# Kernel optimization log

Hardware: AMD Instinct MI355X
Metric: run time of the kernel (lower is better)

## Reference

```python
import jax, jax.numpy as jnp
import numpy as np

NUM_HEADS = 12
HEAD_DIM = 64
DROPKEY = 0.1
BN_EPS = 1e-5


def setup_inputs() -> dict:
    key = jax.random.key(0)
    ks = jax.random.split(key, 6)
    b, n, d = 4, 1024, 768
    img_c, hw = 256, 32
    x = jax.random.normal(ks[0], (b, n, d), dtype=jnp.float32)
    y = jax.random.normal(ks[1], (b, img_c, hw, hw), dtype=jnp.float32)
    drop_mask = jax.random.uniform(ks[2], (b, NUM_HEADS, n, n), dtype=jnp.float32)
    W_qkv = jax.random.normal(ks[3], (d, 3 * d), dtype=jnp.float32) * (d ** -0.5)
    conv1_w = jax.random.normal(ks[4], (img_c, 1, 3, 3), dtype=jnp.float32) * 0.1
    conv2_w = jax.random.normal(ks[5], (d, img_c, 1, 1), dtype=jnp.float32) * (img_c ** -0.5)
    bn_gamma = jnp.ones((d,), dtype=jnp.float32)
    bn_beta = jnp.zeros((d,), dtype=jnp.float32)
    return {"x": x, "y": y, "drop_mask": drop_mask, "W_qkv": W_qkv,
            "conv1_w": conv1_w, "conv2_w": conv2_w,
            "bn_gamma": bn_gamma, "bn_beta": bn_beta}


def reference(x, y, drop_mask, W_qkv, conv1_w, conv2_w, bn_gamma, bn_beta):
    b, n, d = x.shape
    h, hd = NUM_HEADS, HEAD_DIM
    scale = hd ** -0.5

    # --- attention branch ---
    qkv = x @ W_qkv                                     # [b, n, 3d]
    q, k, v = jnp.split(qkv, 3, axis=-1)
    def to_heads(t):
        return t.reshape(b, n, h, hd).transpose(0, 2, 1, 3)  # [b, h, n, hd]
    q, k, v = to_heads(q), to_heads(k), to_heads(v)
    scores = jnp.einsum('bhid,bhjd->bhij', q, k) * scale
    # dropkey: bernoulli(p) additive -1e12 mask before softmax
    mask = (drop_mask < DROPKEY).astype(scores.dtype)
    scores = scores + mask * jnp.asarray(-1e12, scores.dtype)
    attn = jax.nn.softmax(scores, axis=-1)
    out = jnp.einsum('bhij,bhjd->bhid', attn, v)        # [b, h, n, hd]
    out = out.transpose(0, 2, 1, 3).reshape(b, n, h * hd)

    # --- conv branch: depthwise 3x3 -> 1x1 -> BN(train) -> ReLU ---
    img_c = y.shape[1]
    y1 = jax.lax.conv_general_dilated(
        y, conv1_w, window_strides=(1, 1), padding='SAME',
        dimension_numbers=('NCHW', 'OIHW', 'NCHW'),
        feature_group_count=img_c)                      # [b, img_c, H, W]
    y2 = jax.lax.conv_general_dilated(
        y1, conv2_w, window_strides=(1, 1), padding='SAME',
        dimension_numbers=('NCHW', 'OIHW', 'NCHW'))     # [b, d, H, W]
    mean = jnp.mean(y2, axis=(0, 2, 3), keepdims=True)
    var = jnp.var(y2, axis=(0, 2, 3), keepdims=True)
    y_bn = (y2 - mean) * jax.lax.rsqrt(var + BN_EPS)
    y_bn = y_bn * bn_gamma[None, :, None, None] + bn_beta[None, :, None, None]
    y_out = jax.nn.relu(y_bn)                           # [b, d, H, W]

    # patchify(p1=p2=1) + flatten == 'b c h w -> b (h w) c'
    y_tok = y_out.transpose(0, 2, 3, 1).reshape(b, n, d)
    return (out + y_tok, y_out)


if __name__ == '__main__':
    inp = setup_inputs()
    o, yo = jax.jit(reference)(**inp)
    print(o.shape, yo.shape)
```

## Files before the change

kernel.cpp:

```cpp
#include <hip/hip_runtime.h>
#include <cstddef>

#define B_     4
#define NTOK   1024
#define DMODEL 768
#define NH     12
#define IMGC   256
#define NPIX   1024

typedef __attribute__((ext_vector_type(8))) short bf16x8;
typedef __attribute__((ext_vector_type(4))) float f32x4;
typedef __attribute__((ext_vector_type(8))) unsigned short u16x8;

static __device__ __forceinline__ unsigned short f2bf(float f) {
  unsigned int u = __float_as_uint(f);
  u += 0x7FFFu + ((u >> 16) & 1u);
  return (unsigned short)(u >> 16);
}

#define SWZ(row, b) (((row) << 7) + ((b) ^ (((row) & 7) << 4)))

#define GLOAD16(g, l) __builtin_amdgcn_global_load_lds(                      \
    (const __attribute__((address_space(1))) void*)(g),                      \
    (__attribute__((address_space(3))) void*)(l), 16, 0, 0)

__global__ __launch_bounds__(256) void k_cvt(const float* __restrict__ X,
                                             const float* __restrict__ Wqkv,
                                             const float* __restrict__ W2,
                                             const float* __restrict__ Yimg,
                                             const float* __restrict__ w1,
                                             unsigned short* __restrict__ Xb,
                                             unsigned short* __restrict__ Wtb,
                                             unsigned short* __restrict__ W2b,
                                             float* __restrict__ y1,
                                             float* __restrict__ bnacc) {
  __shared__ unsigned short T[32][33];
  const int bid = blockIdx.x;
  const int t = threadIdx.x;
  if (bid < 1536) {
    const size_t i8 = (size_t)bid * 256 + t;
    const float4 a = *(const float4*)(X + i8 * 8);
    const float4 b = *(const float4*)(X + i8 * 8 + 4);
    u16x8 o;
    o[0] = f2bf(a.x); o[1] = f2bf(a.y); o[2] = f2bf(a.z); o[3] = f2bf(a.w);
    o[4] = f2bf(b.x); o[5] = f2bf(b.y); o[6] = f2bf(b.z); o[7] = f2bf(b.w);
    *(u16x8*)(Xb + i8 * 8) = o;
  } else if (bid < 3264) {
    const int b2 = bid - 1536;
    const int n0 = (b2 % 72) * 32, k0 = (b2 / 72) * 32;
    const int tx = t & 31, ty = t >> 5;
#pragma unroll
    for (int i = 0; i < 4; i++) {
      int kl = ty + i * 8;
      T[tx][kl] = f2bf(Wqkv[(size_t)(k0 + kl) * 2304 + n0 + tx]);
    }
    __syncthreads();
#pragma unroll
    for (int i = 0; i < 4; i++) {
      int nl = ty + i * 8;
      Wtb[(size_t)(n0 + nl) * 768 + k0 + tx] = T[nl][tx];
    }
  } else if (bid < 3360) {
    const size_t i8 = (size_t)(bid - 3264) * 256 + t;
    const float4 a = *(const float4*)(W2 + i8 * 8);
    const float4 b = *(const float4*)(W2 + i8 * 8 + 4);
    u16x8 o;
    o[0] = f2bf(a.x); o[1] = f2bf(a.y); o[2] = f2bf(a.z); o[3] = f2bf(a.w);
    o[4] = f2bf(b.x); o[5] = f2bf(b.y); o[6] = f2bf(b.z); o[7] = f2bf(b.w);
    *(u16x8*)(W2b + i8 * 8) = o;
  } else if (bid == 3360) {
    for (int i = t; i < 1536; i += 256) bnacc[i] = 0.0f;
  } else {
    const int bc = bid - 3361;
    const int c = bc & 255;
    const float* yin = Yimg + (size_t)bc * NPIX;
    float* yout = y1 + (size_t)bc * NPIX;
    float w[9];
#pragma unroll
    for (int i = 0; i < 9; i++) w[i] = w1[c * 9 + i];
#pragma unroll
    for (int rep = 0; rep < 4; rep++) {
      int px = t + rep * 256;
      int yy = px >> 5, xx = px & 31;
      float acc = 0.0f;
#pragma unroll
      for (int dy = -1; dy <= 1; dy++) {
        int sy = yy + dy;
        if (sy < 0 || sy > 31) continue;
#pragma unroll
        for (int dx = -1; dx <= 1; dx++) {
          int sx = xx + dx;
          if (sx < 0 || sx > 31) continue;
          acc = fmaf(yin[(sy << 5) + sx], w[(dy + 1) * 3 + dx + 1], acc);
        }
      }
      yout[px] = acc;
    }
  }
}

__global__ __launch_bounds__(256) void k_qkv_gemm(const unsigned short* __restrict__ Xb,
                                                  const unsigned short* __restrict__ Wt,
                                                  unsigned short* __restrict__ q,
                                                  unsigned short* __restrict__ k,
                                                  unsigned short* __restrict__ v) {
  __shared__ __align__(16) char AsB[16384];
  __shared__ __align__(16) char BsB[16384];
  const int t = threadIdx.x;
  const int w = t >> 6, l = t & 63;
  const int r = l & 15, g = l >> 4;
  const int wr = w >> 1, wc = w & 1;
  const int m0 = blockIdx.y * 128;
  const int n0 = blockIdx.x * 128;
  const int rsel  = l >> 3;
  const int slotp = (l & 7) ^ (rsel & 7);
  f32x4 acc[4][4] = {};

  for (int step = 0; step < 12; ++step) {
    const int k0 = step * 64;
#pragma unroll
    for (int i = 0; i < 4; i++) {
      const int chunk = (i << 2) + w;
      const int row = (chunk << 3) + rsel;
      GLOAD16(Xb + (size_t)(m0 + row) * 768 + k0 + (slotp << 3),
              AsB + (chunk << 10) + (l << 4));
      GLOAD16(Wt + (size_t)(n0 + row) * 768 + k0 + (slotp << 3),
              BsB + (chunk << 10) + (l << 4));
    }
    __syncthreads();
#pragma unroll
    for (int kk = 0; kk < 2; kk++) {
      bf16x8 a[4], b[4];
#pragma unroll
      for (int m = 0; m < 4; m++) {
        const int row = wr * 64 + m * 16 + r;
        a[m] = *(const bf16x8*)(AsB + SWZ(row, kk * 64 + (g << 4)));
      }
#pragma unroll
      for (int n = 0; n < 4; n++) {
        const int row = wc * 64 + n * 16 + r;
        b[n] = *(const bf16x8*)(BsB + SWZ(row, kk * 64 + (g << 4)));
      }
#pragma unroll
      for (int m = 0; m < 4; m++)
#pragma unroll
        for (int n = 0; n < 4; n++)
          acc[m][n] = __builtin_amdgcn_mfma_f32_16x16x32_bf16(a[m], b[n], acc[m][n], 0, 0, 0);
    }
    __syncthreads();
  }

  const int which = blockIdx.x / 6;
  const int cbase = (blockIdx.x - which * 6) * 128 + wc * 64;
  unsigned short* dst = which == 0 ? q : (which == 1 ? k : v);
#pragma unroll
  for (int m = 0; m < 4; m++) {
    const int grow = m0 + wr * 64 + m * 16 + g * 4;
#pragma unroll
    for (int n = 0; n < 4; n++) {
      const int c = cbase + n * 16 + r;
      const int head = c >> 6, dim = c & 63;
#pragma unroll
      for (int reg = 0; reg < 4; reg++) {
        const int row = grow + reg;
        const int bb = row >> 10, tok = row & 1023;
        dst[((size_t)(((bb * NH + head) << 10) + tok) << 6) + dim] = f2bf(acc[m][n][reg]);
      }
    }
  }
}

__global__ __launch_bounds__(256) void k_attn(const unsigned short* __restrict__ qb,
                                              const unsigned short* __restrict__ kb,
                                              const unsigned short* __restrict__ vb,
                                              const float* __restrict__ dm,
                                              const float* __restrict__ y2,
                                              const float* __restrict__ bn_sum,
                                              const float* __restrict__ bn_sumsq,
                                              const float* __restrict__ gamma,
                                              const float* __restrict__ beta,
                                              float* __restrict__ out0) {
  __shared__ __align__(16) unsigned short QsA[4096];
  __shared__ __align__(16) unsigned short KsA[4096];
  __shared__ __align__(16) unsigned short VtA[4096];
  __shared__ __align__(16) unsigned short PsA[4096];
  char* qs = (char*)QsA; char* ks = (char*)KsA;
  char* vt = (char*)VtA; char* ps = (char*)PsA;
  const int bh = blockIdx.x;
  const int qt = blockIdx.y;
  const int t  = threadIdx.x;
  const int w = t >> 6, l = t & 63, r = l & 15, g = l >> 4;
  const size_t hbase = (size_t)bh << 16;
  const char* qg = (const char*)(qb + hbase + ((size_t)qt << 12));
  const char* kg = (const char*)(kb + hbase);
  const char* vg = (const char*)(vb + hbase);
  const float* mp = dm + ((size_t)bh << 20) + ((size_t)(qt * 64) << 10);

#pragma unroll
  for (int i = 0; i < 2; i++) {
    int cid = t + (i << 8);
    int row = cid >> 3, slot = cid & 7;
    uint4 val = *(const uint4*)(qg + row * 128 + slot * 16);
    *(uint4*)(qs + SWZ(row, slot * 16)) = val;
  }

  float m_run[4] = {-INFINITY, -INFINITY, -INFINITY, -INFINITY};
  float l_run[4] = {0.0f, 0.0f, 0.0f, 0.0f};
  f32x4 O[4] = {};

  for (int kt = 0; kt < 16; kt++) {
    __syncthreads();
#pragma unroll
    for (int i = 0; i < 2; i++) {
      int cid = t + (i << 8);
      int row = cid >> 3, slot = cid & 7;
      uint4 val = *(const uint4*)(kg + (size_t)(kt * 64 + row) * 128 + slot * 16);
      *(uint4*)(ks + SWZ(row, slot * 16)) = val;
    }
    {
      int j = t & 63, dh = t >> 6;
      const char* vrow = vg + (size_t)(kt * 64 + j) * 128 + dh * 32;
      u16x8 v0 = *(const u16x8*)(vrow);
      u16x8 v1 = *(const u16x8*)(vrow + 16);
#pragma unroll
      for (int e = 0; e < 8; e++) {
        *(unsigned short*)(vt + SWZ(dh * 16 + e, 2 * j))     = v0[e];
        *(unsigned short*)(vt + SWZ(dh * 16 + 8 + e, 2 * j)) = v1[e];
      }
    }
    float md[4][4];
    {
      const float* mr = mp + (size_t)(w * 16 + g * 4) * 1024 + kt * 64 + r;
#pragma unroll
      for (int reg = 0; reg < 4; reg++)
#pragma unroll
        for (int jt = 0; jt < 4; jt++)
          md[reg][jt] = mr[reg * 1024 + jt * 16];
    }
    __syncthreads();

    f32x4 s[4] = {};
    bf16x8 aQ[2];
#pragma unroll
    for (int kc = 0; kc < 2; kc++)
      aQ[kc] = *(const bf16x8*)(qs + SWZ(w * 16 + r, kc * 64 + g * 16));
#pragma unroll
    for (int jt = 0; jt < 4; jt++) {
#pragma unroll
      for (int kc = 0; kc < 2; kc++) {
        bf16x8 bK = *(const bf16x8*)(ks + SWZ(jt * 16 + r, kc * 64 + g * 16));
        s[jt] = __builtin_amdgcn_mfma_f32_16x16x32_bf16(aQ[kc], bK, s[jt], 0, 0, 0);
      }
    }
    float sv[4][4];
#pragma unroll
    for (int jt = 0; jt < 4; jt++)
#pragma unroll
      for (int reg = 0; reg < 4; reg++)
        sv[jt][reg] = s[jt][reg] * 0.125f + (md[reg][jt] < 0.1f ? -1e12f : 0.0f);

    float alpha[4];
#pragma unroll
    for (int reg = 0; reg < 4; reg++) {
      float mt = fmaxf(fmaxf(sv[0][reg], sv[1][reg]), fmaxf(sv[2][reg], sv[3][reg]));
      mt = fmaxf(mt, __shfl_xor(mt, 1));
      mt = fmaxf(mt, __shfl_xor(mt, 2));
      mt = fmaxf(mt, __shfl_xor(mt, 4));
      mt = fmaxf(mt, __shfl_xor(mt, 8));
      float mn = fmaxf(m_run[reg], mt);
      alpha[reg] = __expf(m_run[reg] - mn);
      m_run[reg] = mn;
    }
#pragma unroll
    for (int reg = 0; reg < 4; reg++) {
      int row = w * 16 + g * 4 + reg;
      float ps_ = 0.0f;
#pragma unroll
      for (int jt = 0; jt < 4; jt++) {
        float p = __expf(sv[jt][reg] - m_run[reg]);
        ps_ += p;
        *(unsigned short*)(ps + SWZ(row, 2 * (jt * 16 + r))) = f2bf(p);
      }
      ps_ += __shfl_xor(ps_, 1);
      ps_ += __shfl_xor(ps_, 2);
      ps_ += __shfl_xor(ps_, 4);
      ps_ += __shfl_xor(ps_, 8);
      l_run[reg] = l_run[reg] * alpha[reg] + ps_;
    }
#pragma unroll
    for (int dt = 0; dt < 4; dt++)
#pragma unroll
      for (int reg = 0; reg < 4; reg++)
        O[dt][reg] *= alpha[reg];
    asm volatile("s_waitcnt lgkmcnt(0)" ::: "memory");
    __builtin_amdgcn_sched_barrier(0);
#pragma unroll
    for (int kc = 0; kc < 2; kc++) {
      bf16x8 aP = *(const bf16x8*)(ps + SWZ(w * 16 + r, kc * 64 + g * 16));
#pragma unroll
      for (int dt = 0; dt < 4; dt++) {
        bf16x8 bV = *(const bf16x8*)(vt + SWZ(dt * 16 + r, kc * 64 + g * 16));
        O[dt] = __builtin_amdgcn_mfma_f32_16x16x32_bf16(aP, bV, O[dt], 0, 0, 0);
      }
    }
  }
  const int bb = bh / NH, hh = bh % NH;
  float inv[4];
#pragma unroll
  for (int reg = 0; reg < 4; reg++) inv[reg] = 1.0f / l_run[reg];
  float scv[4], shv[4];
#pragma unroll
  for (int dt = 0; dt < 4; dt++) {
    const int c = hh * 64 + dt * 16 + r;
    const float S = bn_sum[c], SQ = bn_sumsq[c];
    const float mean = S * (1.0f / 4096.0f);
    const float var = SQ * (1.0f / 4096.0f) - mean * mean;
    const float rstd = rsqrtf(var + 1e-5f);
    const float sc = gamma[c] * rstd;
    scv[dt] = sc;
    shv[dt] = fmaf(-mean, sc, beta[c]);
  }
  const int prow = qt * 64 + w * 16 + g * 4;
  const float* y2p = y2 + (((size_t)(bb * DMODEL + hh * 64 + r)) << 10) + prow;
  float4 yq[4];
#pragma unroll
  for (int dt = 0; dt < 4; dt++)
    yq[dt] = *(const float4*)(y2p + ((size_t)dt << 14));
  float* op = out0 + ((size_t)(bb * 1024 + prow)) * 768 + hh * 64 + r;
#pragma unroll
  for (int reg = 0; reg < 4; reg++)
#pragma unroll
    for (int dt = 0; dt < 4; dt++) {
      const float yv = (&yq[dt].x)[reg];
      const float ytok = fmaxf(fmaf(yv, scv[dt], shv[dt]), 0.0f);
      op[(size_t)reg * 768 + dt * 16] = fmaf(O[dt][reg], inv[reg], ytok);
    }
}

__global__ __launch_bounds__(256) void k_trans(const float* __restrict__ y1,
                                               unsigned short* __restrict__ y1t) {
  __shared__ float T[64][65];
  const int p0 = blockIdx.x * 64, c0 = blockIdx.y * 64, b = blockIdx.z;
  const int t = threadIdx.x;
  const float* src = y1 + ((size_t)b << 18);
  {
    const int pl = t & 63, cl0 = t >> 6;
#pragma unroll
    for (int i = 0; i < 16; i++) {
      int cl = cl0 * 16 + i;
      T[cl][pl] = src[(size_t)(c0 + cl) * 1024 + p0 + pl];
    }
  }
  __syncthreads();
  {
    const int cl = t & 63, pl0 = t >> 6;
    unsigned short* dst = y1t + ((size_t)b << 18);
#pragma unroll
    for (int i = 0; i < 16; i++) {
      int pl = pl0 * 16 + i;
      dst[(size_t)(p0 + pl) * 256 + c0 + cl] = f2bf(T[cl][pl]);
    }
  }
}

__global__ __launch_bounds__(256) void k_c1x1(const unsigned short* __restrict__ W2b,
                                              const unsigned short* __restrict__ y1t,
                                              float* __restrict__ Y2,
                                              float* __restrict__ bn_sum,
                                              float* __restrict__ bn_sumsq) {
  __shared__ __align__(16) char AsB[16384];
  __shared__ __align__(16) char BsB[16384];
  const int t = threadIdx.x;
  const int w = t >> 6, l = t & 63;
  const int r = l & 15, g = l >> 4;
  const int wr = w >> 1, wc = w & 1;
  const int m0 = blockIdx.y * 128;
  const int n0 = blockIdx.x * 128;
  const int b  = blockIdx.z;
  const unsigned short* Bb = y1t + ((size_t)b << 18);
  const int rsel  = l >> 3;
  const int slotp = (l & 7) ^ (rsel & 7);
  f32x4 acc[4][4] = {};

  for (int step = 0; step < 4; ++step) {
    const int k0 = step * 64;
#pragma unroll
    for (int i = 0; i < 4; i++) {
      const int chunk = (i << 2) + w;
      const int row = (chunk << 3) + rsel;
      GLOAD16(W2b + (size_t)(m0 + row) * 256 + k0 + (slotp << 3),
              AsB + (chunk << 10) + (l << 4));
      GLOAD16(Bb + (size_t)(n0 + row) * 256 + k0 + (slotp << 3),
              BsB + (chunk << 10) + (l << 4));
    }
    __syncthreads();
#pragma unroll
    for (int kk = 0; kk < 2; kk++) {
      bf16x8 a[4], bfr[4];
#pragma unroll
      for (int m = 0; m < 4; m++) {
        const int row = wr * 64 + m * 16 + r;
        a[m] = *(const bf16x8*)(AsB + SWZ(row, kk * 64 + (g << 4)));
      }
#pragma unroll
      for (int n = 0; n < 4; n++) {
        const int row = wc * 64 + n * 16 + r;
        bfr[n] = *(const bf16x8*)(BsB + SWZ(row, kk * 64 + (g << 4)));
      }
#pragma unroll
      for (int m = 0; m < 4; m++)
#pragma unroll
        for (int n = 0; n < 4; n++)
          acc[m][n] = __builtin_amdgcn_mfma_f32_16x16x32_bf16(a[m], bfr[n], acc[m][n], 0, 0, 0);
    }
    __syncthreads();
  }

  float* Yb = Y2 + (((size_t)b * DMODEL) << 10);
#pragma unroll
  for (int m = 0; m < 4; m++) {
#pragma unroll
    for (int reg = 0; reg < 4; reg++) {
      const int oc = m0 + wr * 64 + m * 16 + g * 4 + reg;
      float s = 0.0f, sq = 0.0f;
#pragma unroll
      for (int n = 0; n < 4; n++) {
        const int p = n0 + wc * 64 + n * 16 + r;
        const float val = acc[m][n][reg];
        Yb[((size_t)oc << 10) + p] = val;
        s += val;
        sq = fmaf(val, val, sq);
      }
      s  += __shfl_xor(s, 1);  sq += __shfl_xor(sq, 1);
      s  += __shfl_xor(s, 2);  sq += __shfl_xor(sq, 2);
      s  += __shfl_xor(s, 4);  sq += __shfl_xor(sq, 4);
      s  += __shfl_xor(s, 8);  sq += __shfl_xor(sq, 8);
      if (r == 0) {
        atomicAdd(&bn_sum[oc], s);
        atomicAdd(&bn_sumsq[oc], sq);
      }
    }
  }
}

__global__ __launch_bounds__(256) void k_bnout1(const float* __restrict__ y2,
                                                const float* __restrict__ bn_sum,
                                                const float* __restrict__ bn_sumsq,
                                                const float* __restrict__ gamma,
                                                const float* __restrict__ beta,
                                                float* __restrict__ out1) {
  const int row = blockIdx.x;
  const int c = row % DMODEL;
  const int t = threadIdx.x;
  const float S = bn_sum[c], SQ = bn_sumsq[c];
  const float mean = S * (1.0f / 4096.0f);
  const float var = SQ * (1.0f / 4096.0f) - mean * mean;
  const float rstd = rsqrtf(var + 1e-5f);
  const float sc = gamma[c] * rstd;
  const float sh = fmaf(-mean, sc, beta[c]);
  const float* src = y2 + ((size_t)row << 10) + t * 4;
  float* dst = out1 + ((size_t)row << 10) + t * 4;
  float4 v = *(const float4*)src;
  v.x = fmaxf(fmaf(v.x, sc, sh), 0.0f);
  v.y = fmaxf(fmaf(v.y, sc, sh), 0.0f);
  v.z = fmaxf(fmaf(v.z, sc, sh), 0.0f);
  v.w = fmaxf(fmaf(v.w, sc, sh), 0.0f);
  *(float4*)dst = v;
}

extern "C" void kernel_launch(void* const* d_in, const int* in_sizes, int n_in,
                              void* d_out, int out_size, void* d_ws, size_t ws_size,
                              hipStream_t stream) {
  (void)in_sizes; (void)n_in; (void)out_size; (void)ws_size;
  const float* x    = (const float*)d_in[0];
  const float* y    = (const float*)d_in[1];
  const float* dm   = (const float*)d_in[2];
  const float* wqkv = (const float*)d_in[3];
  const float* w1   = (const float*)d_in[4];
  const float* w2   = (const float*)d_in[5];
  const float* gam  = (const float*)d_in[6];
  const float* bet  = (const float*)d_in[7];
  float* out0 = (float*)d_out;
  float* out1 = out0 + (size_t)B_ * NTOK * DMODEL;

  char* wsb = (char*)d_ws;
  unsigned short* Xb  = (unsigned short*)wsb;
  unsigned short* Wtb = (unsigned short*)(wsb + 6291456);
  unsigned short* W2b = (unsigned short*)(wsb + 9830400);
  unsigned short* qb  = (unsigned short*)(wsb + 10223616);
  unsigned short* kb  = (unsigned short*)(wsb + 16515072);
  unsigned short* vb  = (unsigned short*)(wsb + 22806528);
  unsigned short* y1t = (unsigned short*)(wsb + 29097984);
  float* y2 = (float*)(wsb + 31195136);
  float* y1 = (float*)(wsb + 35389440);
  float* bnacc = (float*)(wsb + 43778048);
  float* bn_sum = bnacc;
  float* bn_sumsq = bnacc + 768;

  k_cvt<<<dim3(4385), 256, 0, stream>>>(x, wqkv, w2, y, w1, Xb, Wtb, W2b, y1, bnacc);
  k_trans<<<dim3(16, 4, B_), 256, 0, stream>>>(y1, y1t);
  k_c1x1<<<dim3(8, 6, B_), 256, 0, stream>>>(W2b, y1t, y2, bn_sum, bn_sumsq);
  k_qkv_gemm<<<dim3(18, 32), 256, 0, stream>>>(Xb, Wtb, qb, kb, vb);
  k_attn<<<dim3(48, 16), 256, 0, stream>>>(qb, kb, vb, dm, y2, bn_sum, bn_sumsq, gam, bet, out0);
  k_bnout1<<<dim3(B_ * DMODEL), 256, 0, stream>>>(y2, bn_sum, bn_sumsq, gam, bet, out1);
}
```

Measured before the change: 128.0 us.

## Merge QKV and 1x1-conv GEMMs into one launch, fold BN output into attention

The QKV projection GEMM and the 1x1 conv GEMM now run as one kernel, with block index ranges picking which GEMM each block computes (576 QKV blocks plus 192 conv blocks). The standalone BN+ReLU output kernel becomes extra tail blocks of the attention kernel, so the whole pipeline needs two fewer launches. This cuts launch overhead and lets the small conv GEMM fill idle CUs next to the QKV GEMM. The trade-off is that the tail BN blocks queue behind the heavy attention blocks, and both merged kernels now carry the register and LDS footprint of their largest branch.

```diff
diff --git a/kernel.cpp b/kernel.cpp
--- a/kernel.cpp
+++ b/kernel.cpp
@@ -99,72 +99,170 @@
   }
 }
 
-__global__ __launch_bounds__(256) void k_qkv_gemm(const unsigned short* __restrict__ Xb,
-                                                  const unsigned short* __restrict__ Wt,
-                                                  unsigned short* __restrict__ q,
-                                                  unsigned short* __restrict__ k,
-                                                  unsigned short* __restrict__ v) {
+__global__ __launch_bounds__(256) void k_trans(const float* __restrict__ y1,
+                                               unsigned short* __restrict__ y1t) {
+  __shared__ float T[64][65];
+  const int p0 = blockIdx.x * 64, c0 = blockIdx.y * 64, b = blockIdx.z;
+  const int t = threadIdx.x;
+  const float* src = y1 + ((size_t)b << 18);
+  {
+    const int pl = t & 63, cl0 = t >> 6;
+#pragma unroll
+    for (int i = 0; i < 16; i++) {
+      int cl = cl0 * 16 + i;
+      T[cl][pl] = src[(size_t)(c0 + cl) * 1024 + p0 + pl];
+    }
+  }
+  __syncthreads();
+  {
+    const int cl = t & 63, pl0 = t >> 6;
+    unsigned short* dst = y1t + ((size_t)b << 18);
+#pragma unroll
+    for (int i = 0; i < 16; i++) {
+      int pl = pl0 * 16 + i;
+      dst[(size_t)(p0 + pl) * 256 + c0 + cl] = f2bf(T[cl][pl]);
+    }
+  }
+}
+
+__global__ __launch_bounds__(256) void k_mm(const unsigned short* __restrict__ Xb,
+                                            const unsigned short* __restrict__ Wt,
+                                            unsigned short* __restrict__ q,
+                                            unsigned short* __restrict__ k,
+                                            unsigned short* __restrict__ v,
+                                            const unsigned short* __restrict__ W2b,
+                                            const unsigned short* __restrict__ y1t,
+                                            float* __restrict__ Y2,
+                                            float* __restrict__ bn_sum,
+                                            float* __restrict__ bn_sumsq) {
   __shared__ __align__(16) char AsB[16384];
   __shared__ __align__(16) char BsB[16384];
+  const int bid = blockIdx.x;
   const int t = threadIdx.x;
   const int w = t >> 6, l = t & 63;
   const int r = l & 15, g = l >> 4;
   const int wr = w >> 1, wc = w & 1;
-  const int m0 = blockIdx.y * 128;
-  const int n0 = blockIdx.x * 128;
   const int rsel  = l >> 3;
   const int slotp = (l & 7) ^ (rsel & 7);
   f32x4 acc[4][4] = {};
 
-  for (int step = 0; step < 12; ++step) {
-    const int k0 = step * 64;
-#pragma unroll
-    for (int i = 0; i < 4; i++) {
-      const int chunk = (i << 2) + w;
-      const int row = (chunk << 3) + rsel;
-      GLOAD16(Xb + (size_t)(m0 + row) * 768 + k0 + (slotp << 3),
-              AsB + (chunk << 10) + (l << 4));
-      GLOAD16(Wt + (size_t)(n0 + row) * 768 + k0 + (slotp << 3),
-              BsB + (chunk << 10) + (l << 4));
-    }
-    __syncthreads();
-#pragma unroll
-    for (int kk = 0; kk < 2; kk++) {
-      bf16x8 a[4], b[4];
-#pragma unroll
-      for (int m = 0; m < 4; m++) {
-        const int row = wr * 64 + m * 16 + r;
-        a[m] = *(const bf16x8*)(AsB + SWZ(row, kk * 64 + (g << 4)));
-      }
+  if (bid < 576) {
+    const int bx = bid % 18, by = bid / 18;
+    const int m0 = by * 128;
+    const int n0 = bx * 128;
+    for (int step = 0; step < 12; ++step) {
+      const int k0 = step * 64;
+#pragma unroll
+      for (int i = 0; i < 4; i++) {
+        const int chunk = (i << 2) + w;
+        const int row = (chunk << 3) + rsel;
+        GLOAD16(Xb + (size_t)(m0 + row) * 768 + k0 + (slotp << 3),
+                AsB + (chunk << 10) + (l << 4));
+        GLOAD16(Wt + (size_t)(n0 + row) * 768 + k0 + (slotp << 3),
+                BsB + (chunk << 10) + (l << 4));
+      }
+      __syncthreads();
+#pragma unroll
+      for (int kk = 0; kk < 2; kk++) {
+        bf16x8 a[4], b[4];
+#pragma unroll
+        for (int m = 0; m < 4; m++) {
+          const int row = wr * 64 + m * 16 + r;
+          a[m] = *(const bf16x8*)(AsB + SWZ(row, kk * 64 + (g << 4)));
+        }
+#pragma unroll
+        for (int n = 0; n < 4; n++) {
+          const int row = wc * 64 + n * 16 + r;
+          b[n] = *(const bf16x8*)(BsB + SWZ(row, kk * 64 + (g << 4)));
+        }
+#pragma unroll
+        for (int m = 0; m < 4; m++)
+#pragma unroll
+          for (int n = 0; n < 4; n++)
+            acc[m][n] = __builtin_amdgcn_mfma_f32_16x16x32_bf16(a[m], b[n], acc[m][n], 0, 0, 0);
+      }
+      __syncthreads();
+    }
+    const int which = bx / 6;
+    const int cbase = (bx - which * 6) * 128 + wc * 64;
+    unsigned short* dst = which == 0 ? q : (which == 1 ? k : v);
+#pragma unroll
+    for (int m = 0; m < 4; m++) {
+      const int grow = m0 + wr * 64 + m * 16 + g * 4;
 #pragma unroll
       for (int n = 0; n < 4; n++) {
-        const int row = wc * 64 + n * 16 + r;
-        b[n] = *(const bf16x8*)(BsB + SWZ(row, kk * 64 + (g << 4)));
-      }
-#pragma unroll
-      for (int m = 0; m < 4; m++)
-#pragma unroll
-        for (int n = 0; n < 4; n++)
-          acc[m][n] = __builtin_amdgcn_mfma_f32_16x16x32_bf16(a[m], b[n], acc[m][n], 0, 0, 0);
-    }
-    __syncthreads();
-  }
-
-  const int which = blockIdx.x / 6;
-  const int cbase = (blockIdx.x - which * 6) * 128 + wc * 64;
-  unsigned short* dst = which == 0 ? q : (which == 1 ? k : v);
-#pragma unroll
-  for (int m = 0; m < 4; m++) {
-    const int grow = m0 + wr * 64 + m * 16 + g * 4;
-#pragma unroll
-    for (int n = 0; n < 4; n++) {
-      const int c = cbase + n * 16 + r;
-      const int head = c >> 6, dim = c & 63;
+        const int c = cbase + n * 16 + r;
+        const int head = c >> 6, dim = c & 63;
+#pragma unroll
+        for (int reg = 0; reg < 4; reg++) {
+          const int row = grow + reg;
+          const int bb = row >> 10, tok = row & 1023;
+          dst[((size_t)(((bb * NH + head) << 10) + tok) << 6) + dim] = f2bf(acc[m][n][reg]);
+        }
+      }
+    }
+  } else {
+    const int b2 = bid - 576;
+    const int n0 = (b2 & 7) * 128;
+    const int m0 = ((b2 >> 3) % 6) * 128;
+    const int b  = b2 / 48;
+    const unsigned short* Bb = y1t + ((size_t)b << 18);
+    for (int step = 0; step < 4; ++step) {
+      const int k0 = step * 64;
+#pragma unroll
+      for (int i = 0; i < 4; i++) {
+        const int chunk = (i << 2) + w;
+        const int row = (chunk << 3) + rsel;
+        GLOAD16(W2b + (size_t)(m0 + row) * 256 + k0 + (slotp << 3),
+                AsB + (chunk << 10) + (l << 4));
+        GLOAD16(Bb + (size_t)(n0 + row) * 256 + k0 + (slotp << 3),
+                BsB + (chunk << 10) + (l << 4));
+      }
+      __syncthreads();
+#pragma unroll
+      for (int kk = 0; kk < 2; kk++) {
+        bf16x8 a[4], bfr[4];
+#pragma unroll
+        for (int m = 0; m < 4; m++) {
+          const int row = wr * 64 + m * 16 + r;
+          a[m] = *(const bf16x8*)(AsB + SWZ(row, kk * 64 + (g << 4)));
+        }
+#pragma unroll
+        for (int n = 0; n < 4; n++) {
+          const int row = wc * 64 + n * 16 + r;
+          bfr[n] = *(const bf16x8*)(BsB + SWZ(row, kk * 64 + (g << 4)));
+        }
+#pragma unroll
+        for (int m = 0; m < 4; m++)
+#pragma unroll
+          for (int n = 0; n < 4; n++)
+            acc[m][n] = __builtin_amdgcn_mfma_f32_16x16x32_bf16(a[m], bfr[n], acc[m][n], 0, 0, 0);
+      }
+      __syncthreads();
+    }
+    float* Yb = Y2 + (((size_t)b * DMODEL) << 10);
+#pragma unroll
+    for (int m = 0; m < 4; m++) {
 #pragma unroll
       for (int reg = 0; reg < 4; reg++) {
-        const int row = grow + reg;
-        const int bb = row >> 10, tok = row & 1023;
-        dst[((size_t)(((bb * NH + head) << 10) + tok) << 6) + dim] = f2bf(acc[m][n][reg]);
+        const int oc = m0 + wr * 64 + m * 16 + g * 4 + reg;
+        float s = 0.0f, sq = 0.0f;
+#pragma unroll
+        for (int n = 0; n < 4; n++) {
+          const int p = n0 + wc * 64 + n * 16 + r;
+          const float val = acc[m][n][reg];
+          Yb[((size_t)oc << 10) + p] = val;
+          s += val;
+          sq = fmaf(val, val, sq);
+        }
+        s  += __shfl_xor(s, 1);  sq += __shfl_xor(sq, 1);
+        s  += __shfl_xor(s, 2);  sq += __shfl_xor(sq, 2);
+        s  += __shfl_xor(s, 4);  sq += __shfl_xor(sq, 4);
+        s  += __shfl_xor(s, 8);  sq += __shfl_xor(sq, 8);
+        if (r == 0) {
+          atomicAdd(&bn_sum[oc], s);
+          atomicAdd(&bn_sumsq[oc], sq);
+        }
       }
     }
   }
@@ -179,16 +277,37 @@
                                               const float* __restrict__ bn_sumsq,
                                               const float* __restrict__ gamma,
                                               const float* __restrict__ beta,
-                                              float* __restrict__ out0) {
+                                              float* __restrict__ out0,
+                                              float* __restrict__ out1) {
   __shared__ __align__(16) unsigned short QsA[4096];
   __shared__ __align__(16) unsigned short KsA[4096];
   __shared__ __align__(16) unsigned short VtA[4096];
   __shared__ __align__(16) unsigned short PsA[4096];
+  const int bid = blockIdx.x;
+  const int t  = threadIdx.x;
+  if (bid >= 768) {
+    const int row = bid - 768;
+    const int c = row % DMODEL;
+    const float S = bn_sum[c], SQ = bn_sumsq[c];
+    const float mean = S * (1.0f / 4096.0f);
+    const float var = SQ * (1.0f / 4096.0f) - mean * mean;
+    const float rstd = rsqrtf(var + 1e-5f);
+    const float sc = gamma[c] * rstd;
+    const float sh = fmaf(-mean, sc, beta[c]);
+    const float* src = y2 + ((size_t)row << 10) + t * 4;
+    float* dst = out1 + ((size_t)row << 10) + t * 4;
+    float4 vv = *(const float4*)src;
+    vv.x = fmaxf(fmaf(vv.x, sc, sh), 0.0f);
+    vv.y = fmaxf(fmaf(vv.y, sc, sh), 0.0f);
+    vv.z = fmaxf(fmaf(vv.z, sc, sh), 0.0f);
+    vv.w = fmaxf(fmaf(vv.w, sc, sh), 0.0f);
+    *(float4*)dst = vv;
+    return;
+  }
   char* qs = (char*)QsA; char* ks = (char*)KsA;
   char* vt = (char*)VtA; char* ps = (char*)PsA;
-  const int bh = blockIdx.x;
-  const int qt = blockIdx.y;
-  const int t  = threadIdx.x;
+  const int bh = bid % 48;
+  const int qt = bid / 48;
   const int w = t >> 6, l = t & 63, r = l & 15, g = l >> 4;
   const size_t hbase = (size_t)bh << 16;
   const char* qg = (const char*)(qb + hbase + ((size_t)qt << 12));
@@ -335,137 +454,6 @@
       const float ytok = fmaxf(fmaf(yv, scv[dt], shv[dt]), 0.0f);
       op[(size_t)reg * 768 + dt * 16] = fmaf(O[dt][reg], inv[reg], ytok);
     }
-}
-
-__global__ __launch_bounds__(256) void k_trans(const float* __restrict__ y1,
-                                               unsigned short* __restrict__ y1t) {
-  __shared__ float T[64][65];
-  const int p0 = blockIdx.x * 64, c0 = blockIdx.y * 64, b = blockIdx.z;
-  const int t = threadIdx.x;
-  const float* src = y1 + ((size_t)b << 18);
-  {
-    const int pl = t & 63, cl0 = t >> 6;
-#pragma unroll
-    for (int i = 0; i < 16; i++) {
-      int cl = cl0 * 16 + i;
-      T[cl][pl] = src[(size_t)(c0 + cl) * 1024 + p0 + pl];
-    }
-  }
-  __syncthreads();
-  {
-    const int cl = t & 63, pl0 = t >> 6;
-    unsigned short* dst = y1t + ((size_t)b << 18);
-#pragma unroll
-    for (int i = 0; i < 16; i++) {
-      int pl = pl0 * 16 + i;
-      dst[(size_t)(p0 + pl) * 256 + c0 + cl] = f2bf(T[cl][pl]);
-    }
-  }
-}
-
-__global__ __launch_bounds__(256) void k_c1x1(const unsigned short* __restrict__ W2b,
-                                              const unsigned short* __restrict__ y1t,
-                                              float* __restrict__ Y2,
-                                              float* __restrict__ bn_sum,
-                                              float* __restrict__ bn_sumsq) {
-  __shared__ __align__(16) char AsB[16384];
-  __shared__ __align__(16) char BsB[16384];
-  const int t = threadIdx.x;
-  const int w = t >> 6, l = t & 63;
-  const int r = l & 15, g = l >> 4;
-  const int wr = w >> 1, wc = w & 1;
-  const int m0 = blockIdx.y * 128;
-  const int n0 = blockIdx.x * 128;
-  const int b  = blockIdx.z;
-  const unsigned short* Bb = y1t + ((size_t)b << 18);
-  const int rsel  = l >> 3;
-  const int slotp = (l & 7) ^ (rsel & 7);
-  f32x4 acc[4][4] = {};
-
-  for (int step = 0; step < 4; ++step) {
-    const int k0 = step * 64;
-#pragma unroll
-    for (int i = 0; i < 4; i++) {
-      const int chunk = (i << 2) + w;
-      const int row = (chunk << 3) + rsel;
-      GLOAD16(W2b + (size_t)(m0 + row) * 256 + k0 + (slotp << 3),
-              AsB + (chunk << 10) + (l << 4));
-      GLOAD16(Bb + (size_t)(n0 + row) * 256 + k0 + (slotp << 3),
-              BsB + (chunk << 10) + (l << 4));
-    }
-    __syncthreads();
-#pragma unroll
-    for (int kk = 0; kk < 2; kk++) {
-      bf16x8 a[4], bfr[4];
-#pragma unroll
-      for (int m = 0; m < 4; m++) {
-        const int row = wr * 64 + m * 16 + r;
-        a[m] = *(const bf16x8*)(AsB + SWZ(row, kk * 64 + (g << 4)));
-      }
-#pragma unroll
-      for (int n = 0; n < 4; n++) {
-        const int row = wc * 64 + n * 16 + r;
-        bfr[n] = *(const bf16x8*)(BsB + SWZ(row, kk * 64 + (g << 4)));
-      }
-#pragma unroll
-      for (int m = 0; m < 4; m++)
-#pragma unroll
-        for (int n = 0; n < 4; n++)
-          acc[m][n] = __builtin_amdgcn_mfma_f32_16x16x32_bf16(a[m], bfr[n], acc[m][n], 0, 0, 0);
-    }
-    __syncthreads();
-  }
-
-  float* Yb = Y2 + (((size_t)b * DMODEL) << 10);
-#pragma unroll
-  for (int m = 0; m < 4; m++) {
-#pragma unroll
-    for (int reg = 0; reg < 4; reg++) {
-      const int oc = m0 + wr * 64 + m * 16 + g * 4 + reg;
-      float s = 0.0f, sq = 0.0f;
-#pragma unroll
-      for (int n = 0; n < 4; n++) {
-        const int p = n0 + wc * 64 + n * 16 + r;
-        const float val = acc[m][n][reg];
-        Yb[((size_t)oc << 10) + p] = val;
-        s += val;
-        sq = fmaf(val, val, sq);
-      }
-      s  += __shfl_xor(s, 1);  sq += __shfl_xor(sq, 1);
-      s  += __shfl_xor(s, 2);  sq += __shfl_xor(sq, 2);
-      s  += __shfl_xor(s, 4);  sq += __shfl_xor(sq, 4);
-      s  += __shfl_xor(s, 8);  sq += __shfl_xor(sq, 8);
-      if (r == 0) {
-        atomicAdd(&bn_sum[oc], s);
-        atomicAdd(&bn_sumsq[oc], sq);
-      }
-    }
-  }
-}
-
-__global__ __launch_bounds__(256) void k_bnout1(const float* __restrict__ y2,
-                                                const float* __restrict__ bn_sum,
-                                                const float* __restrict__ bn_sumsq,
-                                                const float* __restrict__ gamma,
-                                                const float* __restrict__ beta,
-                                                float* __restrict__ out1) {
-  const int row = blockIdx.x;
-  const int c = row % DMODEL;
-  const int t = threadIdx.x;
-  const float S = bn_sum[c], SQ = bn_sumsq[c];
-  const float mean = S * (1.0f / 4096.0f);
-  const float var = SQ * (1.0f / 4096.0f) - mean * mean;
-  const float rstd = rsqrtf(var + 1e-5f);
-  const float sc = gamma[c] * rstd;
-  const float sh = fmaf(-mean, sc, beta[c]);
-  const float* src = y2 + ((size_t)row << 10) + t * 4;
-  float* dst = out1 + ((size_t)row << 10) + t * 4;
-  float4 v = *(const float4*)src;
-  v.x = fmaxf(fmaf(v.x, sc, sh), 0.0f);
-  v.y = fmaxf(fmaf(v.y, sc, sh), 0.0f);
-  v.z = fmaxf(fmaf(v.z, sc, sh), 0.0f);
-  v.w = fmaxf(fmaf(v.w, sc, sh), 0.0f);
-  *(float4*)dst = v;
 }
 
 extern "C" void kernel_launch(void* const* d_in, const int* in_sizes, int n_in,
@@ -499,8 +487,6 @@
 
   k_cvt<<<dim3(4385), 256, 0, stream>>>(x, wqkv, w2, y, w1, Xb, Wtb, W2b, y1, bnacc);
   k_trans<<<dim3(16, 4, B_), 256, 0, stream>>>(y1, y1t);
-  k_c1x1<<<dim3(8, 6, B_), 256, 0, stream>>>(W2b, y1t, y2, bn_sum, bn_sumsq);
-  k_qkv_gemm<<<dim3(18, 32), 256, 0, stream>>>(Xb, Wtb, qb, kb, vb);
-  k_attn<<<dim3(48, 16), 256, 0, stream>>>(qb, kb, vb, dm, y2, bn_sum, bn_sumsq, gam, bet, out0);
-  k_bnout1<<<dim3(B_ * DMODEL), 256, 0, stream>>>(y2, bn_sum, bn_sumsq, gam, bet, out1);
-}
+  k_mm<<<dim3(768), 256, 0, stream>>>(Xb, Wtb, qb, kb, vb, W2b, y1t, y2, bn_sum, bn_sumsq);
+  k_attn<<<dim3(3840), 256, 0, stream>>>(qb, kb, vb, dm, y2, bn_sum, bn_sumsq, gam, bet, out0, out1);
+}
```

Measured after the change: 122.5 us (median of 2 runs). -4.2%, faster.
